# Optimization experiments

Hardware: AMD Instinct MI355X
Metric: run time of the kernel (lower is better)

## Reference

```python
import jax, jax.numpy as jnp
import numpy as np

B, S, D, H = 2, 2048, 1024, 16
DEPTH = D // H


def setup_inputs() -> dict:
    key = jax.random.key(0)
    ks = jax.random.split(key, 9)
    sc = 1.0 / np.sqrt(D)
    return {
        "x": jax.random.normal(ks[0], (B, S, D), dtype=jnp.float32),
        "wq": jax.random.normal(ks[1], (D, D), dtype=jnp.float32) * sc,
        "bq": jnp.zeros((D,), dtype=jnp.float32),
        "wk": jax.random.normal(ks[2], (D, D), dtype=jnp.float32) * sc,
        "bk": jnp.zeros((D,), dtype=jnp.float32),
        "wv": jax.random.normal(ks[3], (D, D), dtype=jnp.float32) * sc,
        "bv": jnp.zeros((D,), dtype=jnp.float32),
        "wo": jax.random.normal(ks[4], (D, D), dtype=jnp.float32) * sc,
        "bo": jnp.zeros((D,), dtype=jnp.float32),
    }


def _split_heads(t):
    # [B,S,D] -> [B,H,S,depth]
    return t.reshape(B, S, H, DEPTH).transpose(0, 2, 1, 3)


def reference(x, wq, bq, wk, bk, wv, bv, wo, bo):
    q = _split_heads(x @ wq + bq)
    k = _split_heads(x @ wk + bk)
    v = _split_heads(x @ wv + bv)
    scale = 1.0 / jnp.sqrt(jnp.asarray(DEPTH, dtype=x.dtype))
    logits = jnp.einsum("bhqd,bhkd->bhqk", q, k) * scale
    attn = jax.nn.relu(logits)  # ReLU replaces softmax
    ctx = jnp.einsum("bhqk,bhkd->bhqd", attn, v)
    concat = ctx.transpose(0, 2, 1, 3).reshape(B, S, D)
    out = concat @ wo + bo
    return out, attn
```

## Files before the change

### kernel.cpp

```cpp
#include <hip/hip_runtime.h>
#include <hip/hip_bf16.h>

constexpr int Bn = 2, Sn = 2048, Dn = 1024, Hn = 16, DEP = 64;
constexpr int NTOKn = Bn * Sn;

typedef __bf16 bf16x8 __attribute__((ext_vector_type(8)));
typedef float f32x4 __attribute__((ext_vector_type(4)));

__device__ __forceinline__ unsigned short f2bf(float f) {
    union { __hip_bfloat16 h; unsigned short u; } cv;
    cv.h = __float2bfloat16(f);
    return cv.u;
}

__device__ __forceinline__ void gll16(const void* g, void* l) {
    __builtin_amdgcn_global_load_lds(
        (const __attribute__((address_space(1))) unsigned int*)g,
        (__attribute__((address_space(3))) unsigned int*)l, 16, 0, 0);
}

__global__ __launch_bounds__(256) void k_cvt_x(const float* __restrict__ x,
                                               unsigned short* __restrict__ xb,
                                               int n) {
    int idx = (blockIdx.x * 256 + threadIdx.x) * 4;
    if (idx < n) {
        float4 v = *reinterpret_cast<const float4*>(x + idx);
        ushort4 o;
        o.x = f2bf(v.x); o.y = f2bf(v.y); o.z = f2bf(v.z); o.w = f2bf(v.w);
        *reinterpret_cast<ushort4*>(xb + idx) = o;
    }
}

__global__ __launch_bounds__(256) void k_tconv_w(const float* __restrict__ w0,
                                                 const float* __restrict__ w1,
                                                 const float* __restrict__ w2,
                                                 const float* __restrict__ w3,
                                                 unsigned short* __restrict__ t0,
                                                 unsigned short* __restrict__ t1,
                                                 unsigned short* __restrict__ t2,
                                                 unsigned short* __restrict__ t3) {
    const float* w; unsigned short* tp;
    switch (blockIdx.z) {
        case 0: w = w0; tp = t0; break;
        case 1: w = w1; tp = t1; break;
        case 2: w = w2; tp = t2; break;
        default: w = w3; tp = t3; break;
    }
    __shared__ unsigned short tile[64][65];
    const int k0 = blockIdx.x * 64, n0 = blockIdx.y * 64;
    const int t = threadIdx.x;
    const int c = t & 63, rb = t >> 6;
#pragma unroll
    for (int i = 0; i < 16; ++i) {
        int r = rb + i * 4;
        tile[r][c] = f2bf(w[(size_t)(k0 + r) * Dn + n0 + c]);
    }
    __syncthreads();
#pragma unroll
    for (int i = 0; i < 16; ++i) {
        int n = rb + i * 4;
        tp[(size_t)(n0 + n) * Dn + k0 + c] = tile[c][n];
    }
}

__global__ __launch_bounds__(256) void k_tr_v(const unsigned short* __restrict__ V,
                                              unsigned short* __restrict__ VT) {
    __shared__ unsigned short tile[64][65];
    const int s0 = blockIdx.x * 64;
    const int bh = blockIdx.y;
    const int b = bh >> 4, h = bh & 15;
    const int t = threadIdx.x;
    const int c = t & 63, rb = t >> 6;
#pragma unroll
    for (int i = 0; i < 16; ++i) {
        int r = rb + i * 4;
        tile[r][c] = V[(size_t)(b * Sn + s0 + r) * Dn + h * DEP + c];
    }
    __syncthreads();
#pragma unroll
    for (int i = 0; i < 16; ++i) {
        int d = rb + i * 4;
        VT[(size_t)(bh * DEP + d) * Sn + s0 + c] = tile[c][d];
    }
}

template <bool OUT_F32, bool QKV3>
__global__ __launch_bounds__(256) void k_gemm(const unsigned short* __restrict__ A,
                                              const unsigned short* __restrict__ Bt_,
                                              const float* __restrict__ b0,
                                              const float* __restrict__ b1,
                                              const float* __restrict__ b2,
                                              void* __restrict__ C_,
                                              int M, int N, int K) {
    __shared__ unsigned short As[128][32];
    __shared__ unsigned short Bs[128][32];
    const int t = threadIdx.x;
    const int w = t >> 6, l = t & 63;
    const int m0 = blockIdx.x * 128, n0 = blockIdx.y * 128;
    const int wr = (w >> 1) * 64, wc = (w & 1) * 64;

    const unsigned short* Bt = Bt_;
    const float* bias = b0;
    char* Cb = (char*)C_;
    if (QKV3) {
        const int z = blockIdx.z;
        Bt = Bt_ + (size_t)z * N * K;
        bias = (z == 0) ? b0 : (z == 1 ? b1 : b2);
        Cb = (char*)C_ + (size_t)z * M * N * (OUT_F32 ? 4 : 2);
    }

    const int lrow = t >> 2;
    const int lcol = (t & 3) * 8;
    const unsigned short* gA = A + (size_t)(m0 + lrow) * K + lcol;
    const unsigned short* gB = Bt + (size_t)(n0 + lrow) * K + lcol;
    unsigned short* lA = &As[0][0] + t * 8;
    unsigned short* lB = &Bs[0][0] + t * 8;

    f32x4 acc[4][4] = {};

    for (int k0 = 0; k0 < K; k0 += 32) {
        __syncthreads();
        gll16(gA + k0, lA);
        gll16(gA + (size_t)64 * K + k0, lA + 2048);
        gll16(gB + k0, lB);
        gll16(gB + (size_t)64 * K + k0, lB + 2048);
        __syncthreads();

        bf16x8 af[4], bfv[4];
#pragma unroll
        for (int i = 0; i < 4; ++i)
            af[i] = *reinterpret_cast<const bf16x8*>(&As[wr + i * 16 + (l & 15)][(l >> 4) * 8]);
#pragma unroll
        for (int i = 0; i < 4; ++i)
            bfv[i] = *reinterpret_cast<const bf16x8*>(&Bs[wc + i * 16 + (l & 15)][(l >> 4) * 8]);
#pragma unroll
        for (int mi = 0; mi < 4; ++mi)
#pragma unroll
            for (int ni = 0; ni < 4; ++ni)
                acc[mi][ni] =
                    __builtin_amdgcn_mfma_f32_16x16x32_bf16(af[mi], bfv[ni], acc[mi][ni], 0, 0, 0);
    }

#pragma unroll
    for (int mi = 0; mi < 4; ++mi) {
        const int row = m0 + wr + mi * 16 + (l >> 4) * 4;
#pragma unroll
        for (int ni = 0; ni < 4; ++ni) {
            const int col = n0 + wc + ni * 16 + (l & 15);
            const float bv = bias[col];
#pragma unroll
            for (int i = 0; i < 4; ++i) {
                const float v = acc[mi][ni][i] + bv;
                if (OUT_F32)
                    reinterpret_cast<float*>(Cb)[(size_t)(row + i) * N + col] = v;
                else
                    reinterpret_cast<unsigned short*>(Cb)[(size_t)(row + i) * N + col] = f2bf(v);
            }
        }
    }
}

__global__ __launch_bounds__(256, 2) void k_attn(const unsigned short* __restrict__ Qb,
                                                 const unsigned short* __restrict__ Kb,
                                                 const unsigned short* __restrict__ VTb,
                                                 float* __restrict__ attn,
                                                 unsigned short* __restrict__ ctx) {
    __shared__ unsigned short Ks[128 * 64];
    __shared__ unsigned short Vs[64 * 128];
    __shared__ unsigned short Ps[4][32][136];

    const int t = threadIdx.x;
    const int w = t >> 6, l = t & 63;
    const int q0 = blockIdx.x * 128;
    const int bh = blockIdx.y;
    const int b = bh >> 4, h = bh & 15;
    const float scale = 0.125f;

    bf16x8 qf[2][2];
#pragma unroll
    for (int mi = 0; mi < 2; ++mi)
#pragma unroll
        for (int kk = 0; kk < 2; ++kk)
            qf[mi][kk] = *reinterpret_cast<const bf16x8*>(
                Qb + (size_t)(b * Sn + q0 + w * 32 + mi * 16 + (l & 15)) * Dn + h * DEP +
                kk * 32 + (l >> 4) * 8);

    const int krow = t >> 3;
    const int kcolswz = ((t & 7) * 8) ^ ((krow & 7) << 3);
    const int vrow = t >> 4;
    const int vcolswz = ((t & 15) * 8) ^ ((vrow & 7) << 3);
    unsigned short* lK = Ks + t * 8;
    unsigned short* lV = Vs + t * 8;

    f32x4 ctxa[2][4] = {};

    for (int kb = 0; kb < Sn / 128; ++kb) {
        __syncthreads();
#pragma unroll
        for (int is = 0; is < 4; ++is) {
            gll16(Kb + (size_t)(b * Sn + kb * 128 + is * 32 + krow) * Dn + h * DEP + kcolswz,
                  lK + is * 2048);
            gll16(VTb + (size_t)(bh * DEP + is * 16 + vrow) * Sn + kb * 128 + vcolswz,
                  lV + is * 2048);
        }
        __syncthreads();

        f32x4 sa[2][8] = {};
#pragma unroll
        for (int nj = 0; nj < 8; ++nj) {
            const int kr = nj * 16 + (l & 15);
#pragma unroll
            for (int kk = 0; kk < 2; ++kk) {
                const int kidx = (kr * 64 + kk * 32 + (l >> 4) * 8) ^ ((kr & 7) << 3);
                const bf16x8 bfr = *reinterpret_cast<const bf16x8*>(Ks + kidx);
                sa[0][nj] = __builtin_amdgcn_mfma_f32_16x16x32_bf16(qf[0][kk], bfr, sa[0][nj], 0, 0, 0);
                sa[1][nj] = __builtin_amdgcn_mfma_f32_16x16x32_bf16(qf[1][kk], bfr, sa[1][nj], 0, 0, 0);
            }
        }

        float* arow = attn + (size_t)bh * Sn * Sn + (size_t)q0 * Sn + (size_t)kb * 128;
#pragma unroll
        for (int mi = 0; mi < 2; ++mi) {
#pragma unroll
            for (int nj = 0; nj < 8; ++nj) {
                const int kc = nj * 16 + (l & 15);
#pragma unroll
                for (int i = 0; i < 4; ++i) {
                    const int qr = w * 32 + mi * 16 + (l >> 4) * 4 + i;
                    float p = sa[mi][nj][i] * scale;
                    p = p > 0.f ? p : 0.f;
                    arow[(size_t)qr * Sn + kc] = p;
                    Ps[w][qr & 31][kc] = f2bf(p);
                }
            }
        }
        __syncthreads();

        bf16x8 pf[2][4];
#pragma unroll
        for (int mi = 0; mi < 2; ++mi)
#pragma unroll
            for (int kk = 0; kk < 4; ++kk)
                pf[mi][kk] = *reinterpret_cast<const bf16x8*>(
                    &Ps[w][mi * 16 + (l & 15)][kk * 32 + (l >> 4) * 8]);
#pragma unroll
        for (int nd = 0; nd < 4; ++nd) {
            const int vr = nd * 16 + (l & 15);
#pragma unroll
            for (int kk = 0; kk < 4; ++kk) {
                const int vidx = (vr * 128 + kk * 32 + (l >> 4) * 8) ^ ((vr & 7) << 3);
                const bf16x8 vfr = *reinterpret_cast<const bf16x8*>(Vs + vidx);
                ctxa[0][nd] = __builtin_amdgcn_mfma_f32_16x16x32_bf16(pf[0][kk], vfr, ctxa[0][nd], 0, 0, 0);
                ctxa[1][nd] = __builtin_amdgcn_mfma_f32_16x16x32_bf16(pf[1][kk], vfr, ctxa[1][nd], 0, 0, 0);
            }
        }
    }

#pragma unroll
    for (int mi = 0; mi < 2; ++mi) {
#pragma unroll
        for (int nd = 0; nd < 4; ++nd) {
            const int dc = nd * 16 + (l & 15);
#pragma unroll
            for (int i = 0; i < 4; ++i) {
                const int qr = q0 + w * 32 + mi * 16 + (l >> 4) * 4 + i;
                ctx[(size_t)(b * Sn + qr) * Dn + h * DEP + dc] = f2bf(ctxa[mi][nd][i]);
            }
        }
    }
}

extern "C" void kernel_launch(void* const* d_in, const int* in_sizes, int n_in,
                              void* d_out, int out_size, void* d_ws, size_t ws_size,
                              hipStream_t stream) {
    (void)in_sizes; (void)n_in; (void)out_size; (void)ws_size;
    const float* x  = (const float*)d_in[0];
    const float* wq = (const float*)d_in[1];
    const float* bq = (const float*)d_in[2];
    const float* wk = (const float*)d_in[3];
    const float* bk = (const float*)d_in[4];
    const float* wv = (const float*)d_in[5];
    const float* bv = (const float*)d_in[6];
    const float* wo = (const float*)d_in[7];
    const float* bo = (const float*)d_in[8];

    float* out  = (float*)d_out;
    float* attn = out + (size_t)Bn * Sn * Dn;

    char* ws = (char*)d_ws;
    unsigned short* xb = (unsigned short*)ws;  ws += (size_t)NTOKn * Dn * 2;
    unsigned short* wT = (unsigned short*)ws;  ws += (size_t)4 * Dn * Dn * 2;
    unsigned short* qkv = (unsigned short*)ws; ws += (size_t)3 * NTOKn * Dn * 2;
    unsigned short* vT = (unsigned short*)ws;  ws += (size_t)NTOKn * Dn * 2;
    unsigned short* ctx = (unsigned short*)ws;

    const size_t DD = (size_t)Dn * Dn;

    k_cvt_x<<<dim3(NTOKn * Dn / 4 / 256), 256, 0, stream>>>(x, xb, NTOKn * Dn);
    k_tconv_w<<<dim3(16, 16, 4), 256, 0, stream>>>(wq, wk, wv, wo,
                                                   wT, wT + DD, wT + 2 * DD, wT + 3 * DD);
    k_gemm<false, true><<<dim3(32, 8, 3), 256, 0, stream>>>(xb, wT, bq, bk, bv, qkv,
                                                            NTOKn, Dn, Dn);
    k_tr_v<<<dim3(32, 32), 256, 0, stream>>>(qkv + (size_t)2 * NTOKn * Dn, vT);
    k_attn<<<dim3(16, 32), 256, 0, stream>>>(qkv, qkv + (size_t)NTOKn * Dn, vT, attn, ctx);
    k_gemm<true, false><<<dim3(32, 8, 1), 256, 0, stream>>>(ctx, wT + 3 * DD, bo, bo, bo,
                                                            out, NTOKn, Dn, Dn);
}
```

Baseline: 228.7 us.

## Defer attention-score stores to overlap with the next K/V tile load

Splits the attention loop body into stage, QK^T, PV and store phases. The fp32 attention-score stores for block kb-1 are issued right after the async K/V loads for block kb, so the two overlap. A partial vmcnt wait (63) then waits only for the older loads and not for the 64 pending stores per thread. The per-iteration __syncthreads calls become raw s_barrier plus manual waitcnt, with sched_barrier fences. This relies on exact counter arithmetic and keeps the sa registers live across phases, which may raise register pressure.

Result: faster. 224.0 us (-2.0%).

```diff
diff --git a/kernel.cpp b/kernel.cpp
--- a/kernel.cpp
+++ b/kernel.cpp
@@ -193,9 +193,11 @@
     unsigned short* lV = Vs + t * 8;
 
     f32x4 ctxa[2][4] = {};
-
-    for (int kb = 0; kb < Sn / 128; ++kb) {
-        __syncthreads();
+    f32x4 sa[2][8];
+
+    float* const abase = attn + (size_t)bh * Sn * Sn + (size_t)(q0 + w * 32) * Sn;
+
+    auto STAGE = [&](int kb) {
 #pragma unroll
         for (int is = 0; is < 4; ++is) {
             gll16(Kb + (size_t)(b * Sn + kb * 128 + is * 32 + krow) * Dn + h * DEP + kcolswz,
@@ -203,9 +205,14 @@
             gll16(VTb + (size_t)(bh * DEP + is * 16 + vrow) * Sn + kb * 128 + vcolswz,
                   lV + is * 2048);
         }
-        __syncthreads();
-
-        f32x4 sa[2][8] = {};
+    };
+
+    auto QKT = [&]() {
+#pragma unroll
+        for (int mi = 0; mi < 2; ++mi)
+#pragma unroll
+            for (int nj = 0; nj < 8; ++nj)
+                sa[mi][nj] = (f32x4){0.f, 0.f, 0.f, 0.f};
 #pragma unroll
         for (int nj = 0; nj < 8; ++nj) {
             const int kr = nj * 16 + (l & 15);
@@ -217,25 +224,26 @@
                 sa[1][nj] = __builtin_amdgcn_mfma_f32_16x16x32_bf16(qf[1][kk], bfr, sa[1][nj], 0, 0, 0);
             }
         }
-
-        float* arow = attn + (size_t)bh * Sn * Sn + (size_t)q0 * Sn + (size_t)kb * 128;
 #pragma unroll
         for (int mi = 0; mi < 2; ++mi) {
 #pragma unroll
             for (int nj = 0; nj < 8; ++nj) {
+                f32x4 v = sa[mi][nj];
+#pragma unroll
+                for (int i = 0; i < 4; ++i) {
+                    float p = v[i] * scale;
+                    v[i] = p > 0.f ? p : 0.f;
+                }
+                sa[mi][nj] = v;
                 const int kc = nj * 16 + (l & 15);
 #pragma unroll
-                for (int i = 0; i < 4; ++i) {
-                    const int qr = w * 32 + mi * 16 + (l >> 4) * 4 + i;
-                    float p = sa[mi][nj][i] * scale;
-                    p = p > 0.f ? p : 0.f;
-                    arow[(size_t)qr * Sn + kc] = p;
-                    Ps[w][qr & 31][kc] = f2bf(p);
-                }
-            }
-        }
-        __syncthreads();
-
+                for (int i = 0; i < 4; ++i)
+                    Ps[w][mi * 16 + (l >> 4) * 4 + i][kc] = f2bf(v[i]);
+            }
+        }
+    };
+
+    auto PV = [&]() {
         bf16x8 pf[2][4];
 #pragma unroll
         for (int mi = 0; mi < 2; ++mi)
@@ -254,7 +262,42 @@
                 ctxa[1][nd] = __builtin_amdgcn_mfma_f32_16x16x32_bf16(pf[1][kk], vfr, ctxa[1][nd], 0, 0, 0);
             }
         }
-    }
+    };
+
+    auto STORE_SA = [&](int kb) {
+        float* arow = abase + kb * 128;
+#pragma unroll
+        for (int mi = 0; mi < 2; ++mi)
+#pragma unroll
+            for (int nj = 0; nj < 8; ++nj) {
+                const int kc = nj * 16 + (l & 15);
+#pragma unroll
+                for (int i = 0; i < 4; ++i)
+                    arow[(size_t)(mi * 16 + (l >> 4) * 4 + i) * Sn + kc] = sa[mi][nj][i];
+            }
+    };
+
+    STAGE(0);
+    asm volatile("s_waitcnt vmcnt(0)" ::: "memory");
+    __builtin_amdgcn_s_barrier();
+    __builtin_amdgcn_sched_barrier(0);
+    QKT();
+    PV();
+
+    for (int kb = 1; kb < Sn / 128; ++kb) {
+        asm volatile("s_waitcnt lgkmcnt(0)" ::: "memory");
+        __builtin_amdgcn_s_barrier();
+        __builtin_amdgcn_sched_barrier(0);
+        STAGE(kb);
+        asm volatile("" ::: "memory");
+        STORE_SA(kb - 1);
+        asm volatile("s_waitcnt vmcnt(63)" ::: "memory");
+        __builtin_amdgcn_s_barrier();
+        __builtin_amdgcn_sched_barrier(0);
+        QKT();
+        PV();
+    }
+    STORE_SA(Sn / 128 - 1);
 
 #pragma unroll
     for (int mi = 0; mi < 2; ++mi) {
```
